# Performance work log

Measured on AMD Instinct MI355X. Metric: run time of the kernel, lower is better.

Reference implementation:

```python
import jax, jax.numpy as jnp
import numpy as np

N_AGENTS, OBS_DIM, HID, ACT_DIM = 8192, 64, 128, 16


def setup_inputs() -> dict:
    key = jax.random.key(0)
    k = jax.random.split(key, 8)
    obs_agents = jax.random.normal(k[0], (N_AGENTS, OBS_DIM), dtype=jnp.float32)
    # binary adjacency, {0,1}, int32 (index/mask semantics, non-differentiable)
    adj = jax.random.randint(k[1], (N_AGENTS, N_AGENTS), 0, 2, dtype=jnp.int32)
    def lin(kk, fan_in, fan_out):
        lim = 1.0 / np.sqrt(fan_in)
        kw, kb = jax.random.split(kk)
        W = jax.random.uniform(kw, (fan_in, fan_out), jnp.float32, -lim, lim)
        b = jax.random.uniform(kb, (fan_out,), jnp.float32, -lim, lim)
        return W, b
    W1, b1 = lin(k[2], OBS_DIM, HID)          # encoder
    W2, b2 = lin(k[3], 2 * HID, HID)          # actor layer 1
    W3, b3 = lin(k[4], HID, ACT_DIM)          # actor layer 2
    return {"obs_agents": obs_agents, "adj": adj,
            "W1": W1, "b1": b1, "W2": W2, "b2": b2, "W3": W3, "b3": b3}


def reference(obs_agents, adj, W1, b1, W2, b2, W3, b3):
    # per-agent encode: h = tanh(obs @ W1 + b1)  -> [N, HID]
    h = jnp.tanh(obs_agents @ W1 + b1)
    # neighbor mean message: mean of h[j] over j with adj[i,j]!=0, zeros if no neighbors
    a = adj.astype(h.dtype)                      # [N, N] binary
    deg = jnp.sum(a, axis=1, keepdims=True)      # [N, 1]
    msg = (a @ h) / jnp.maximum(deg, 1.0)        # zero rows stay zero
    # actor MLP on concat([h, msg])
    combined = jnp.concatenate([h, msg], axis=-1)            # [N, 2*HID]
    hid = jnp.tanh(combined @ W2 + b2)                        # [N, HID]
    logits = hid @ W3 + b3                                    # [N, ACT_DIM]
    return logits
```

## Files before the change

### kernel.cpp

```cpp
#include <hip/hip_runtime.h>
#include <stdint.h>
#include <math.h>

#define NAG 8192
#define NB  144
#define NSPLIT 8
#define LDB 264

typedef __attribute__((ext_vector_type(8))) short short8;
typedef __attribute__((ext_vector_type(4))) float floatx4;

__device__ __forceinline__ float bf2f(unsigned short u) {
    union { uint32_t i; float f; } v; v.i = ((uint32_t)u) << 16; return v.f;
}
__device__ __forceinline__ unsigned short f2bf(float f) {
    union { float f; uint32_t i; } v; v.f = f;
    uint32_t x = v.i;
    return (unsigned short)((x + 0x7FFFu + ((x >> 16) & 1u)) >> 16);
}
__device__ __forceinline__ unsigned short f2h(float f) {
    union { _Float16 h; unsigned short u; } v; v.h = (_Float16)f; return v.u;
}
__device__ __forceinline__ float h2f(unsigned short u) {
    union { _Float16 h; unsigned short u; } v; v.u = u; return (float)v.h;
}

__global__ __launch_bounds__(64) void k0_init(
    int* __restrict__ flag, const unsigned short* __restrict__ W1raw)
{
    int big = 0;
    #pragma unroll
    for (int j = 0; j < 8; ++j) {
        float v = bf2f(W1raw[threadIdx.x * 8 + j]);
        if (!(fabsf(v) <= 1e6f)) big = 1;
    }
    unsigned long long m = __ballot(big);
    if (threadIdx.x == 0) *flag = (m != 0ull) ? 1 : 0;
}

__global__ __launch_bounds__(256) void kp_pack(
    const int* __restrict__ adj, unsigned long long* __restrict__ bits)
{
    const int lane = threadIdx.x & 63;
    const int gw = blockIdx.x * 4 + (threadIdx.x >> 6);
    for (int it = 0; it < 32; ++it) {
        size_t u = ((size_t)it * 8192 + gw) * 4;
        size_t col = u * 64 + lane;
        unsigned long long m0, m1, m2, m3;
        m0 = __ballot(adj[col]         != 0);
        m1 = __ballot(adj[col + 64]    != 0);
        m2 = __ballot(adj[col + 128]   != 0);
        m3 = __ballot(adj[col + 192]   != 0);
        if (lane == 0) {
            bits[u]     = m0;
            bits[u + 1] = m1;
            bits[u + 2] = m2;
            bits[u + 3] = m3;
        }
    }
}

__global__ __launch_bounds__(256) void k1_encode(
    const void* __restrict__ obs,
    const void* __restrict__ W1,
    const void* __restrict__ b1,
    const int* __restrict__ flag,
    float* __restrict__ h_f32,
    unsigned short* __restrict__ hT)
{
    __shared__ float obs_lds[32][68];
    __shared__ unsigned short ht_lds[128][33];
    const int t = threadIdx.x;
    const int abase = blockIdx.x * 32;
    const bool isf = (*flag != 0);

    {
        int a = t >> 3, c0 = (t & 7) * 8;
        if (isf) {
            const float* p = (const float*)obs;
            #pragma unroll
            for (int j = 0; j < 8; ++j)
                obs_lds[a][c0 + j] = p[(size_t)(abase + a) * 64 + c0 + j];
        } else {
            const unsigned short* p = (const unsigned short*)obs;
            #pragma unroll
            for (int j = 0; j < 8; ++j)
                obs_lds[a][c0 + j] = bf2f(p[(size_t)(abase + a) * 64 + c0 + j]);
        }
    }
    __syncthreads();

    const int o = t & 127;
    const int half = t >> 7;
    float acc[16];
    if (isf) {
        const float* Wp = (const float*)W1;
        float bias = ((const float*)b1)[o];
        #pragma unroll
        for (int i = 0; i < 16; ++i) acc[i] = bias;
        for (int k0 = 0; k0 < 64; k0 += 8) {
            float w[8];
            #pragma unroll
            for (int j = 0; j < 8; ++j) w[j] = Wp[(k0 + j) * 128 + o];
            #pragma unroll
            for (int j = 0; j < 8; ++j)
                #pragma unroll
                for (int i = 0; i < 16; ++i)
                    acc[i] = fmaf(obs_lds[half * 16 + i][k0 + j], w[j], acc[i]);
        }
    } else {
        const unsigned short* Wp = (const unsigned short*)W1;
        float bias = bf2f(((const unsigned short*)b1)[o]);
        #pragma unroll
        for (int i = 0; i < 16; ++i) acc[i] = bias;
        for (int k0 = 0; k0 < 64; k0 += 8) {
            float w[8];
            #pragma unroll
            for (int j = 0; j < 8; ++j) w[j] = bf2f(Wp[(k0 + j) * 128 + o]);
            #pragma unroll
            for (int j = 0; j < 8; ++j)
                #pragma unroll
                for (int i = 0; i < 16; ++i)
                    acc[i] = fmaf(obs_lds[half * 16 + i][k0 + j], w[j], acc[i]);
        }
    }
    #pragma unroll
    for (int i = 0; i < 16; ++i) {
        float th = tanhf(acc[i]);
        int a = half * 16 + i;
        h_f32[(size_t)(abase + a) * 128 + o] = th;
        ht_lds[o][a] = f2bf(th);
    }
    __syncthreads();

    for (int p = 0; p < 18; ++p) {
        int n = p * 8 + (t >> 5);
        int a = t & 31;
        unsigned short v;
        if (n < 128)       v = ht_lds[n][a];
        else if (n == 128) v = 0x3F80;
        else               v = 0;
        hT[(size_t)n * NAG + abase + a] = v;
    }
}

__global__ __launch_bounds__(256, 2) void k2_msggemm(
    const uint32_t* __restrict__ bits,
    const unsigned short* __restrict__ hT,
    unsigned short* __restrict__ Cp16)
{
    __shared__ __align__(16) unsigned short Blds[144 * LDB];
    const int t = threadIdx.x;
    const int mtile = blockIdx.x & 127;
    const int ks = blockIdx.x >> 7;
    const int row0 = mtile * 64;
    const int kbeg = ks * 1024;

    const int wave = t >> 6, lane = t & 63;
    const int fm = lane & 15, quad = lane >> 4;

    floatx4 acc[9];
    #pragma unroll
    for (int i = 0; i < 9; ++i) acc[i] = (floatx4)0.f;

    const int arow = row0 + wave * 16 + fm;
    const uint32_t* aWp = bits + (size_t)arow * 256 + (kbeg >> 5);

    for (int ss = 0; ss < 4; ++ss) {
        if (ss) __syncthreads();
        #pragma unroll 9
        for (int i = 0; i < 18; ++i) {
            int idx = i * 256 + t;
            int row = idx >> 5, ch = idx & 31;
            uint4 v = *reinterpret_cast<const uint4*>(hT + (size_t)row * NAG + kbeg + ss * 256 + ch * 8);
            *reinterpret_cast<uint4*>(&Blds[row * LDB + ch * 8]) = v;
        }
        int4 a0 = *reinterpret_cast<const int4*>(aWp + ss * 8);
        int4 a1 = *reinterpret_cast<const int4*>(aWp + ss * 8 + 4);
        uint32_t aw[8] = {(uint32_t)a0.x, (uint32_t)a0.y, (uint32_t)a0.z, (uint32_t)a0.w,
                          (uint32_t)a1.x, (uint32_t)a1.y, (uint32_t)a1.z, (uint32_t)a1.w};
        __syncthreads();
        #pragma unroll
        for (int kw = 0; kw < 8; ++kw) {
            uint32_t b = (aw[kw] >> (quad * 8)) & 0xFFu;
            union { uint32_t u[4]; short8 s; } af;
            #pragma unroll
            for (int p = 0; p < 4; ++p) {
                uint32_t bb = b >> (2 * p);
                af.u[p] = ((bb & 1u) | ((bb & 2u) << 15)) * 0x3F80u;
            }
            #pragma unroll
            for (int j = 0; j < 9; ++j) {
                short8 bf = *reinterpret_cast<const short8*>(&Blds[(j * 16 + fm) * LDB + kw * 32 + quad * 8]);
                acc[j] = __builtin_amdgcn_mfma_f32_16x16x32_bf16(af.s, bf, acc[j], 0, 0, 0);
            }
        }
    }

    unsigned short* out = Cp16 + (size_t)ks * (NAG * NB);
    #pragma unroll
    for (int j = 0; j < 9; ++j) {
        int col = j * 16 + fm;
        #pragma unroll
        for (int r = 0; r < 4; ++r) {
            int row = row0 + wave * 16 + quad * 4 + r;
            out[(size_t)row * NB + col] = f2h(acc[j][r]);
        }
    }
}

__global__ __launch_bounds__(256) void k3_actor(
    const float* __restrict__ h_f32,
    const unsigned short* __restrict__ Cp16,
    const void* __restrict__ W2,
    const void* __restrict__ b2,
    const void* __restrict__ W3,
    const void* __restrict__ b3,
    const int* __restrict__ flag,
    void* __restrict__ out)
{
    __shared__ float4 comb4[16][66];
    __shared__ float hid[16][132];
    __shared__ float inv_lds[16];
    const int t = threadIdx.x;
    const int abase = blockIdx.x * 16;
    const bool isf = (*flag != 0);
    const size_t PS = (size_t)NAG * NB;

    if (t < 16) {
        float deg = 0.f;
        #pragma unroll
        for (int s = 0; s < NSPLIT; ++s)
            deg += h2f(Cp16[s * PS + (size_t)(abase + t) * NB + 128]);
        inv_lds[t] = 1.0f / fmaxf(deg, 1.0f);
    }
    __syncthreads();

    #pragma unroll
    for (int jj = 0; jj < 4; ++jj) {
        int idx = jj * 256 + t;
        int a = idx >> 6, q = idx & 63;
        float4 v;
        if (q < 32) {
            v = *reinterpret_cast<const float4*>(h_f32 + (size_t)(abase + a) * 128 + q * 4);
        } else {
            int f = (q - 32) * 4;
            float s0 = 0.f, s1 = 0.f, s2 = 0.f, s3 = 0.f;
            #pragma unroll
            for (int s = 0; s < NSPLIT; ++s) {
                ushort4 p = *reinterpret_cast<const ushort4*>(Cp16 + s * PS + (size_t)(abase + a) * NB + f);
                s0 += h2f(p.x); s1 += h2f(p.y); s2 += h2f(p.z); s3 += h2f(p.w);
            }
            float sc = inv_lds[a];
            v = make_float4(s0 * sc, s1 * sc, s2 * sc, s3 * sc);
        }
        comb4[a][q] = v;
    }
    __syncthreads();

    const int o = t & 127, half = t >> 7;
    float acc[8];
    if (isf) {
        const float* Wp = (const float*)W2;
        float bias = ((const float*)b2)[o];
        #pragma unroll
        for (int i = 0; i < 8; ++i) acc[i] = bias;
        for (int cq = 0; cq < 64; ++cq) {
            float w0 = Wp[(cq * 4 + 0) * 128 + o];
            float w1 = Wp[(cq * 4 + 1) * 128 + o];
            float w2 = Wp[(cq * 4 + 2) * 128 + o];
            float w3 = Wp[(cq * 4 + 3) * 128 + o];
            #pragma unroll
            for (int i = 0; i < 8; ++i) {
                float4 v = comb4[half * 8 + i][cq];
                acc[i] = fmaf(v.x, w0, acc[i]);
                acc[i] = fmaf(v.y, w1, acc[i]);
                acc[i] = fmaf(v.z, w2, acc[i]);
                acc[i] = fmaf(v.w, w3, acc[i]);
            }
        }
    } else {
        const unsigned short* Wp = (const unsigned short*)W2;
        float bias = bf2f(((const unsigned short*)b2)[o]);
        #pragma unroll
        for (int i = 0; i < 8; ++i) acc[i] = bias;
        for (int cq = 0; cq < 64; ++cq) {
            float w0 = bf2f(Wp[(cq * 4 + 0) * 128 + o]);
            float w1 = bf2f(Wp[(cq * 4 + 1) * 128 + o]);
            float w2 = bf2f(Wp[(cq * 4 + 2) * 128 + o]);
            float w3 = bf2f(Wp[(cq * 4 + 3) * 128 + o]);
            #pragma unroll
            for (int i = 0; i < 8; ++i) {
                float4 v = comb4[half * 8 + i][cq];
                acc[i] = fmaf(v.x, w0, acc[i]);
                acc[i] = fmaf(v.y, w1, acc[i]);
                acc[i] = fmaf(v.z, w2, acc[i]);
                acc[i] = fmaf(v.w, w3, acc[i]);
            }
        }
    }
    #pragma unroll
    for (int i = 0; i < 8; ++i)
        hid[half * 8 + i][o] = tanhf(acc[i]);
    __syncthreads();

    const int q = t & 15, ar = t >> 4;
    float l;
    if (isf) {
        const float* Wp = (const float*)W3;
        l = ((const float*)b3)[q];
        #pragma unroll 4
        for (int oo = 0; oo < 128; ++oo)
            l = fmaf(hid[ar][oo], Wp[oo * 16 + q], l);
    } else {
        const unsigned short* Wp = (const unsigned short*)W3;
        l = bf2f(((const unsigned short*)b3)[q]);
        #pragma unroll 4
        for (int oo = 0; oo < 128; ++oo)
            l = fmaf(hid[ar][oo], bf2f(Wp[oo * 16 + q]), l);
    }
    size_t i0 = (size_t)(abase + ar) * 16 + q;
    if (isf) ((float*)out)[i0] = l;
    else     ((unsigned short*)out)[i0] = f2bf(l);
}

extern "C" void kernel_launch(void* const* d_in, const int* in_sizes, int n_in,
                              void* d_out, int out_size, void* d_ws, size_t ws_size,
                              hipStream_t stream) {
    const void* obs = d_in[0];
    const int*  adj = (const int*)d_in[1];
    const void* W1  = d_in[2];
    const void* b1  = d_in[3];
    const void* W2  = d_in[4];
    const void* b2  = d_in[5];
    const void* W3  = d_in[6];
    const void* b3  = d_in[7];

    char* ws = (char*)d_ws;
    unsigned short* hT   = (unsigned short*)(ws);
    float*          h_f32= (float*)(ws + 2359296);
    unsigned short* Cp16 = (unsigned short*)(ws + 6553600);
    unsigned long long* bits = (unsigned long long*)(ws + 25427968);
    int*            flag = (int*)(ws + 33816576);

    hipLaunchKernelGGL(k0_init, dim3(1), dim3(64), 0, stream, flag, (const unsigned short*)W1);
    hipLaunchKernelGGL(kp_pack, dim3(2048), dim3(256), 0, stream, adj, bits);
    hipLaunchKernelGGL(k1_encode, dim3(256), dim3(256), 0, stream, obs, W1, b1, flag, h_f32, hT);
    hipLaunchKernelGGL(k2_msggemm, dim3(1024), dim3(256), 0, stream,
                       (const uint32_t*)bits, hT, Cp16);
    hipLaunchKernelGGL(k3_actor, dim3(512), dim3(256), 0, stream, h_f32, Cp16, W2, b2, W3, b3, flag, d_out);
}
```

Measured before the change: 459.6 us.

## Merge init/pack/encode kernels, shrink GEMM K-stage, halve actor tile

Removes the flag-init kernel by having each block detect the input dtype inline, and fuses the adjacency bit-pack and encoder into one launch split by block index. The message GEMM now stages 128 columns per step instead of 256, halving LDS use so launch bounds can request 4 blocks per CU. The actor kernel processes 8 agents per block instead of 16, doubling the grid. These aim to cut launch overhead and raise occupancy, at the cost of more barriers and redundant weight loads per block.

Measured after the change: 434.9 us. 1.06x faster.

```diff
diff --git a/kernel.cpp b/kernel.cpp
--- a/kernel.cpp
+++ b/kernel.cpp
@@ -5,7 +5,7 @@
 #define NAG 8192
 #define NB  144
 #define NSPLIT 8
-#define LDB 264
+#define LDB2 136
 
 typedef __attribute__((ext_vector_type(8))) short short8;
 typedef __attribute__((ext_vector_type(4))) float floatx4;
@@ -24,55 +24,50 @@
 __device__ __forceinline__ float h2f(unsigned short u) {
     union { _Float16 h; unsigned short u; } v; v.u = u; return (float)v.h;
 }
-
-__global__ __launch_bounds__(64) void k0_init(
-    int* __restrict__ flag, const unsigned short* __restrict__ W1raw)
-{
-    int big = 0;
+__device__ __forceinline__ bool detect_f32(const void* W1, int t) {
+    const unsigned short* w = (const unsigned short*)W1;
+    int l = t & 63, big = 0;
     #pragma unroll
     for (int j = 0; j < 8; ++j) {
-        float v = bf2f(W1raw[threadIdx.x * 8 + j]);
+        float v = bf2f(w[l * 8 + j]);
         if (!(fabsf(v) <= 1e6f)) big = 1;
     }
-    unsigned long long m = __ballot(big);
-    if (threadIdx.x == 0) *flag = (m != 0ull) ? 1 : 0;
-}
-
-__global__ __launch_bounds__(256) void kp_pack(
-    const int* __restrict__ adj, unsigned long long* __restrict__ bits)
-{
-    const int lane = threadIdx.x & 63;
-    const int gw = blockIdx.x * 4 + (threadIdx.x >> 6);
-    for (int it = 0; it < 32; ++it) {
-        size_t u = ((size_t)it * 8192 + gw) * 4;
-        size_t col = u * 64 + lane;
-        unsigned long long m0, m1, m2, m3;
-        m0 = __ballot(adj[col]         != 0);
-        m1 = __ballot(adj[col + 64]    != 0);
-        m2 = __ballot(adj[col + 128]   != 0);
-        m3 = __ballot(adj[col + 192]   != 0);
-        if (lane == 0) {
-            bits[u]     = m0;
-            bits[u + 1] = m1;
-            bits[u + 2] = m2;
-            bits[u + 3] = m3;
-        }
-    }
-}
-
-__global__ __launch_bounds__(256) void k1_encode(
+    return __ballot(big) != 0ull;
+}
+
+__global__ __launch_bounds__(256) void kA_pack_encode(
+    const int* __restrict__ adj,
+    unsigned long long* __restrict__ bits,
     const void* __restrict__ obs,
     const void* __restrict__ W1,
     const void* __restrict__ b1,
-    const int* __restrict__ flag,
     float* __restrict__ h_f32,
     unsigned short* __restrict__ hT)
 {
+    const int t = threadIdx.x;
+    if (blockIdx.x < 2048) {
+        const int lane = t & 63;
+        const int gw = blockIdx.x * 4 + (t >> 6);
+        for (int it = 0; it < 32; ++it) {
+            size_t u = ((size_t)it * 8192 + gw) * 4;
+            size_t col = u * 64 + lane;
+            unsigned long long m0 = __ballot(adj[col]       != 0);
+            unsigned long long m1 = __ballot(adj[col + 64]  != 0);
+            unsigned long long m2 = __ballot(adj[col + 128] != 0);
+            unsigned long long m3 = __ballot(adj[col + 192] != 0);
+            if (lane == 0) {
+                bits[u]     = m0;
+                bits[u + 1] = m1;
+                bits[u + 2] = m2;
+                bits[u + 3] = m3;
+            }
+        }
+        return;
+    }
     __shared__ float obs_lds[32][68];
     __shared__ unsigned short ht_lds[128][33];
-    const int t = threadIdx.x;
-    const int abase = blockIdx.x * 32;
-    const bool isf = (*flag != 0);
+    const int abase = (blockIdx.x - 2048) * 32;
+    const bool isf = detect_f32(W1, t);
 
     {
         int a = t >> 3, c0 = (t & 7) * 8;
@@ -144,12 +139,12 @@
     }
 }
 
-__global__ __launch_bounds__(256, 2) void k2_msggemm(
+__global__ __launch_bounds__(256, 4) void k2_msggemm(
     const uint32_t* __restrict__ bits,
     const unsigned short* __restrict__ hT,
     unsigned short* __restrict__ Cp16)
 {
-    __shared__ __align__(16) unsigned short Blds[144 * LDB];
+    __shared__ __align__(16) unsigned short Blds[144 * LDB2];
     const int t = threadIdx.x;
     const int mtile = blockIdx.x & 127;
     const int ks = blockIdx.x >> 7;
@@ -166,22 +161,20 @@
     const int arow = row0 + wave * 16 + fm;
     const uint32_t* aWp = bits + (size_t)arow * 256 + (kbeg >> 5);
 
-    for (int ss = 0; ss < 4; ++ss) {
+    for (int ss = 0; ss < 8; ++ss) {
         if (ss) __syncthreads();
-        #pragma unroll 9
-        for (int i = 0; i < 18; ++i) {
+        #pragma unroll
+        for (int i = 0; i < 9; ++i) {
             int idx = i * 256 + t;
-            int row = idx >> 5, ch = idx & 31;
-            uint4 v = *reinterpret_cast<const uint4*>(hT + (size_t)row * NAG + kbeg + ss * 256 + ch * 8);
-            *reinterpret_cast<uint4*>(&Blds[row * LDB + ch * 8]) = v;
-        }
-        int4 a0 = *reinterpret_cast<const int4*>(aWp + ss * 8);
-        int4 a1 = *reinterpret_cast<const int4*>(aWp + ss * 8 + 4);
-        uint32_t aw[8] = {(uint32_t)a0.x, (uint32_t)a0.y, (uint32_t)a0.z, (uint32_t)a0.w,
-                          (uint32_t)a1.x, (uint32_t)a1.y, (uint32_t)a1.z, (uint32_t)a1.w};
+            int row = idx >> 4, ch = idx & 15;
+            uint4 v = *reinterpret_cast<const uint4*>(hT + (size_t)row * NAG + kbeg + ss * 128 + ch * 8);
+            *reinterpret_cast<uint4*>(&Blds[row * LDB2 + ch * 8]) = v;
+        }
+        int4 a0 = *reinterpret_cast<const int4*>(aWp + ss * 4);
+        uint32_t aw[4] = {(uint32_t)a0.x, (uint32_t)a0.y, (uint32_t)a0.z, (uint32_t)a0.w};
         __syncthreads();
         #pragma unroll
-        for (int kw = 0; kw < 8; ++kw) {
+        for (int kw = 0; kw < 4; ++kw) {
             uint32_t b = (aw[kw] >> (quad * 8)) & 0xFFu;
             union { uint32_t u[4]; short8 s; } af;
             #pragma unroll
@@ -191,7 +184,7 @@
             }
             #pragma unroll
             for (int j = 0; j < 9; ++j) {
-                short8 bf = *reinterpret_cast<const short8*>(&Blds[(j * 16 + fm) * LDB + kw * 32 + quad * 8]);
+                short8 bf = *reinterpret_cast<const short8*>(&Blds[(j * 16 + fm) * LDB2 + kw * 32 + quad * 8]);
                 acc[j] = __builtin_amdgcn_mfma_f32_16x16x32_bf16(af.s, bf, acc[j], 0, 0, 0);
             }
         }
@@ -212,22 +205,22 @@
 __global__ __launch_bounds__(256) void k3_actor(
     const float* __restrict__ h_f32,
     const unsigned short* __restrict__ Cp16,
+    const void* __restrict__ W1,
     const void* __restrict__ W2,
     const void* __restrict__ b2,
     const void* __restrict__ W3,
     const void* __restrict__ b3,
-    const int* __restrict__ flag,
     void* __restrict__ out)
 {
-    __shared__ float4 comb4[16][66];
-    __shared__ float hid[16][132];
-    __shared__ float inv_lds[16];
+    __shared__ float4 comb4[8][66];
+    __shared__ float hid[8][132];
+    __shared__ float inv_lds[8];
     const int t = threadIdx.x;
-    const int abase = blockIdx.x * 16;
-    const bool isf = (*flag != 0);
+    const int abase = blockIdx.x * 8;
+    const bool isf = detect_f32(W1, t);
     const size_t PS = (size_t)NAG * NB;
 
-    if (t < 16) {
+    if (t < 8) {
         float deg = 0.f;
         #pragma unroll
         for (int s = 0; s < NSPLIT; ++s)
@@ -237,7 +230,7 @@
     __syncthreads();
 
     #pragma unroll
-    for (int jj = 0; jj < 4; ++jj) {
+    for (int jj = 0; jj < 2; ++jj) {
         int idx = jj * 256 + t;
         int a = idx >> 6, q = idx & 63;
         float4 v;
@@ -259,20 +252,20 @@
     __syncthreads();
 
     const int o = t & 127, half = t >> 7;
-    float acc[8];
+    float acc[4];
     if (isf) {
         const float* Wp = (const float*)W2;
         float bias = ((const float*)b2)[o];
         #pragma unroll
-        for (int i = 0; i < 8; ++i) acc[i] = bias;
+        for (int i = 0; i < 4; ++i) acc[i] = bias;
         for (int cq = 0; cq < 64; ++cq) {
             float w0 = Wp[(cq * 4 + 0) * 128 + o];
             float w1 = Wp[(cq * 4 + 1) * 128 + o];
             float w2 = Wp[(cq * 4 + 2) * 128 + o];
             float w3 = Wp[(cq * 4 + 3) * 128 + o];
             #pragma unroll
-            for (int i = 0; i < 8; ++i) {
-                float4 v = comb4[half * 8 + i][cq];
+            for (int i = 0; i < 4; ++i) {
+                float4 v = comb4[half * 4 + i][cq];
                 acc[i] = fmaf(v.x, w0, acc[i]);
                 acc[i] = fmaf(v.y, w1, acc[i]);
                 acc[i] = fmaf(v.z, w2, acc[i]);
@@ -283,15 +276,15 @@
         const unsigned short* Wp = (const unsigned short*)W2;
         float bias = bf2f(((const unsigned short*)b2)[o]);
         #pragma unroll
-        for (int i = 0; i < 8; ++i) acc[i] = bias;
+        for (int i = 0; i < 4; ++i) acc[i] = bias;
         for (int cq = 0; cq < 64; ++cq) {
             float w0 = bf2f(Wp[(cq * 4 + 0) * 128 + o]);
             float w1 = bf2f(Wp[(cq * 4 + 1) * 128 + o]);
             float w2 = bf2f(Wp[(cq * 4 + 2) * 128 + o]);
             float w3 = bf2f(Wp[(cq * 4 + 3) * 128 + o]);
             #pragma unroll
-            for (int i = 0; i < 8; ++i) {
-                float4 v = comb4[half * 8 + i][cq];
+            for (int i = 0; i < 4; ++i) {
+                float4 v = comb4[half * 4 + i][cq];
                 acc[i] = fmaf(v.x, w0, acc[i]);
                 acc[i] = fmaf(v.y, w1, acc[i]);
                 acc[i] = fmaf(v.z, w2, acc[i]);
@@ -300,28 +293,30 @@
         }
     }
     #pragma unroll
-    for (int i = 0; i < 8; ++i)
-        hid[half * 8 + i][o] = tanhf(acc[i]);
-    __syncthreads();
-
-    const int q = t & 15, ar = t >> 4;
-    float l;
-    if (isf) {
-        const float* Wp = (const float*)W3;
-        l = ((const float*)b3)[q];
-        #pragma unroll 4
-        for (int oo = 0; oo < 128; ++oo)
-            l = fmaf(hid[ar][oo], Wp[oo * 16 + q], l);
-    } else {
-        const unsigned short* Wp = (const unsigned short*)W3;
-        l = bf2f(((const unsigned short*)b3)[q]);
-        #pragma unroll 4
-        for (int oo = 0; oo < 128; ++oo)
-            l = fmaf(hid[ar][oo], bf2f(Wp[oo * 16 + q]), l);
-    }
-    size_t i0 = (size_t)(abase + ar) * 16 + q;
-    if (isf) ((float*)out)[i0] = l;
-    else     ((unsigned short*)out)[i0] = f2bf(l);
+    for (int i = 0; i < 4; ++i)
+        hid[half * 4 + i][o] = tanhf(acc[i]);
+    __syncthreads();
+
+    if (t < 128) {
+        const int q = t & 15, ar = t >> 4;
+        float l;
+        if (isf) {
+            const float* Wp = (const float*)W3;
+            l = ((const float*)b3)[q];
+            #pragma unroll 4
+            for (int oo = 0; oo < 128; ++oo)
+                l = fmaf(hid[ar][oo], Wp[oo * 16 + q], l);
+        } else {
+            const unsigned short* Wp = (const unsigned short*)W3;
+            l = bf2f(((const unsigned short*)b3)[q]);
+            #pragma unroll 4
+            for (int oo = 0; oo < 128; ++oo)
+                l = fmaf(hid[ar][oo], bf2f(Wp[oo * 16 + q]), l);
+        }
+        size_t i0 = (size_t)(abase + ar) * 16 + q;
+        if (isf) ((float*)out)[i0] = l;
+        else     ((unsigned short*)out)[i0] = f2bf(l);
+    }
 }
 
 extern "C" void kernel_launch(void* const* d_in, const int* in_sizes, int n_in,
@@ -341,12 +336,11 @@
     float*          h_f32= (float*)(ws + 2359296);
     unsigned short* Cp16 = (unsigned short*)(ws + 6553600);
     unsigned long long* bits = (unsigned long long*)(ws + 25427968);
-    int*            flag = (int*)(ws + 33816576);
-
-    hipLaunchKernelGGL(k0_init, dim3(1), dim3(64), 0, stream, flag, (const unsigned short*)W1);
-    hipLaunchKernelGGL(kp_pack, dim3(2048), dim3(256), 0, stream, adj, bits);
-    hipLaunchKernelGGL(k1_encode, dim3(256), dim3(256), 0, stream, obs, W1, b1, flag, h_f32, hT);
+
+    hipLaunchKernelGGL(kA_pack_encode, dim3(2304), dim3(256), 0, stream,
+                       adj, bits, obs, W1, b1, h_f32, hT);
     hipLaunchKernelGGL(k2_msggemm, dim3(1024), dim3(256), 0, stream,
                        (const uint32_t*)bits, hT, Cp16);
-    hipLaunchKernelGGL(k3_actor, dim3(512), dim3(256), 0, stream, h_f32, Cp16, W2, b2, W3, b3, flag, d_out);
-}
+    hipLaunchKernelGGL(k3_actor, dim3(1024), dim3(256), 0, stream,
+                       h_f32, Cp16, W1, W2, b2, W3, b3, d_out);
+}
```
